# Performance work log

Measured on AMD Instinct MI355X. Metric: run time of the kernel, lower is better.

The kernel has to match this reference:

```python
import jax, jax.numpy as jnp
import numpy as np

LN_EPS = 1e-5


def setup_inputs() -> dict:
    key = jax.random.key(0)
    ks = jax.random.split(key, 10)
    N, E, D, H = 32000, 512000, 256, 128
    atom_features = jax.random.normal(ks[0], (N, D), dtype=jnp.float32)
    edge_features = jax.random.normal(ks[1], (E, H), dtype=jnp.float32)
    edge_index = jax.random.randint(ks[2], (2, E), 0, N, dtype=jnp.int64)
    s = lambda fan_in: 1.0 / np.sqrt(fan_in)
    W_lin = jax.random.normal(ks[3], (D, H), dtype=jnp.float32) * s(D)
    W1 = jax.random.normal(ks[4], (3 * H, H), dtype=jnp.float32) * s(3 * H)
    b1 = jnp.zeros((H,), jnp.float32)
    W2 = jax.random.normal(ks[5], (H, H), dtype=jnp.float32) * s(H)
    b2 = jnp.zeros((H,), jnp.float32)
    W3 = jax.random.normal(ks[6], (H, H), dtype=jnp.float32) * s(H)
    b3 = jnp.zeros((H,), jnp.float32)
    gamma = jnp.ones((H,), jnp.float32)
    beta = jnp.zeros((H,), jnp.float32)
    return dict(atom_features=atom_features, edge_features=edge_features,
                edge_index=edge_index, W_lin=W_lin, W1=W1, b1=b1, W2=W2,
                b2=b2, W3=W3, b3=b3, gamma=gamma, beta=beta)


def _layernorm(x, gamma, beta):
    mu = jnp.mean(x, axis=-1, keepdims=True)
    var = jnp.mean((x - mu) ** 2, axis=-1, keepdims=True)
    return (x - mu) * jax.lax.rsqrt(var + LN_EPS) * gamma + beta


def reference(atom_features, edge_features, edge_index, W_lin, W1, b1, W2, b2, W3, b3, gamma, beta):
    # o3.Linear on scalar irreps -> plain bias-free linear: [N, D] @ [D, H]
    atom_scalars = atom_features @ W_lin  # [N, H]
    edge_dst, edge_src = edge_index[0], edge_index[1]
    # gather + concat: [E, 3H]
    edge_in = jnp.concatenate(
        [atom_scalars[edge_dst], atom_scalars[edge_src], edge_features], axis=-1)
    h = jax.nn.relu(edge_in @ W1 + b1)
    h = jax.nn.relu(h @ W2 + b2)
    h = h @ W3 + b3  # [E, H]
    return _layernorm(edge_features + h, gamma, beta)
```

## Files before the change

kernel.cpp:

```cpp
#include <hip/hip_runtime.h>

typedef __attribute__((ext_vector_type(8))) short bf16x8;
typedef __attribute__((ext_vector_type(16))) float f32x16;
typedef __attribute__((ext_vector_type(4))) float f32x4;
typedef __attribute__((ext_vector_type(4))) unsigned u32x4;

#define LN_EPS 1e-5f

__device__ __forceinline__ unsigned short f2bf(float f) {
    unsigned u = __float_as_uint(f);
    unsigned r = (u + 0x7FFFu + ((u >> 16) & 1u)) >> 16;
    return (unsigned short)r;
}

__device__ __forceinline__ unsigned cvt_pk_bf16(float lo, float hi) {
    unsigned r;
    asm("v_cvt_pk_bf16_f32 %0, %1, %2" : "=v"(r) : "v"(lo), "v"(hi));
    return r;
}

__device__ __forceinline__ void permswap(unsigned& a, unsigned& b) {
    asm("v_permlane32_swap_b32 %0, %1" : "+v"(a), "+v"(b));
}

__global__ void prep_weights(const float* __restrict__ W_lin,
                             const float* __restrict__ W1,
                             const float* __restrict__ W2,
                             const float* __restrict__ W3,
                             unsigned short* __restrict__ wt_lin,
                             unsigned short* __restrict__ wimg) {
    int i = blockIdx.x * blockDim.x + threadIdx.x;
    if (i < 128 * 256) {
        int n = i >> 8, k = i & 255;
        wt_lin[n * 256 + k] = f2bf(W_lin[k * 128 + n]);
    } else if (i < 128 * 256 + 5 * 16384) {
        int j = i - 128 * 256;
        int mat = j >> 14, r = j & 16383;
        int jj = r & 7, l = (r >> 3) & 63, ks = (r >> 9) & 7, f = r >> 12;
        int n = 32 * f + (l & 31);
        int k = 16 * ks + 8 * (l >> 5) + jj;
        float v;
        if (mat < 3)       v = W1[(mat * 128 + k) * 128 + n];
        else if (mat == 3) v = W2[k * 128 + n];
        else               v = W3[k * 128 + n];
        wimg[j] = f2bf(v);
    }
}

__global__ void atoms_gemm(const float* __restrict__ af,
                           const unsigned short* __restrict__ wt_lin,
                           unsigned short* __restrict__ atoms_bf,
                           int Natoms) {
    const int wv = threadIdx.x >> 6, lane = threadIdx.x & 63;
    const int l31 = lane & 31, g8 = (lane >> 5) * 8, g4 = (lane >> 5) * 4;
    const int R = blockIdx.x * 128 + wv * 32;

    f32x16 acc[4];
#pragma unroll
    for (int f = 0; f < 4; ++f)
#pragma unroll
        for (int e = 0; e < 16; ++e) acc[f][e] = 0.0f;

    int arow = R + l31;
    if (arow >= Natoms) arow = Natoms - 1;
    const float* ap = af + (size_t)arow * 256;

#pragma unroll
    for (int ks = 0; ks < 16; ++ks) {
        const int k0 = ks * 16 + g8;
        float4 x0 = *(const float4*)(ap + k0);
        float4 x1 = *(const float4*)(ap + k0 + 4);
        bf16x8 a;
        a[0] = (short)f2bf(x0.x); a[1] = (short)f2bf(x0.y);
        a[2] = (short)f2bf(x0.z); a[3] = (short)f2bf(x0.w);
        a[4] = (short)f2bf(x1.x); a[5] = (short)f2bf(x1.y);
        a[6] = (short)f2bf(x1.z); a[7] = (short)f2bf(x1.w);
#pragma unroll
        for (int f = 0; f < 4; ++f) {
            bf16x8 b = *(const bf16x8*)(wt_lin + (32 * f + l31) * 256 + k0);
            acc[f] = __builtin_amdgcn_mfma_f32_32x32x16_bf16(a, b, acc[f], 0, 0, 0);
        }
    }

#pragma unroll
    for (int f = 0; f < 4; ++f) {
        const int col = 32 * f + l31;
#pragma unroll
        for (int r = 0; r < 16; ++r) {
            int row = R + (r & 3) + 8 * (r >> 2) + g4;
            if (row < Natoms) atoms_bf[(size_t)row * 128 + col] = f2bf(acc[f][r]);
        }
    }
}

__global__ __launch_bounds__(512, 2) void edge_fused(
    const float* __restrict__ ef, const int* __restrict__ eidx,
    const unsigned short* __restrict__ atoms_bf,
    const unsigned short* __restrict__ wimg,
    const float* __restrict__ b1, const float* __restrict__ b2,
    const float* __restrict__ b3, const float* __restrict__ gamma_,
    const float* __restrict__ beta_, float* __restrict__ out, int E) {
    __shared__ unsigned short wlds[4 * 16384];

    const int tid = threadIdx.x;
    const int lane = tid & 63, wv = tid >> 6;
    const int l31 = lane & 31, hi = lane >> 5, h8 = hi * 8;

    {
        const char* s = (const char*)wimg;
        char* d = (char*)wlds;
        const int o = tid * 16;
#pragma unroll
        for (int i = 0; i < 16; ++i)
            __builtin_amdgcn_global_load_lds(
                (const __attribute__((address_space(1))) unsigned int*)(s + o + i * 8192),
                (__attribute__((address_space(3))) unsigned int*)(d + o + i * 8192),
                16, 0, 0);
    }

    const int e0a = blockIdx.x * 512 + wv * 64 + l31;
    const int e0b = e0a + 32;
    const int ea = e0a < E ? e0a : E - 1;
    const int eb = e0b < E ? e0b : E - 1;
    const int dA = eidx[ea], sA = eidx[E + ea];
    const int dB = eidx[eb], sB = eidx[E + eb];
    const unsigned short* dRowA = atoms_bf + (size_t)dA * 128;
    const unsigned short* sRowA = atoms_bf + (size_t)sA * 128;
    const unsigned short* dRowB = atoms_bf + (size_t)dB * 128;
    const unsigned short* sRowB = atoms_bf + (size_t)sB * 128;
    const float* efA = ef + (size_t)ea * 128;
    const float* efB = ef + (size_t)eb * 128;

    bf16x8 gdA[8], gdB[8];
#pragma unroll
    for (int ks = 0; ks < 8; ++ks) {
        gdA[ks] = *(const bf16x8*)(dRowA + ks * 16 + h8);
        gdB[ks] = *(const bf16x8*)(dRowB + ks * 16 + h8);
    }

    f32x16 accA[4], accB[4];
    auto initb = [&](const float* __restrict__ bb) {
#pragma unroll
        for (int f = 0; f < 4; ++f)
#pragma unroll
            for (int m = 0; m < 4; ++m) {
                f32x4 b4 = *(const f32x4*)(bb + 32 * f + 8 * m + 4 * hi);
#pragma unroll
                for (int i = 0; i < 4; ++i) {
                    accA[f][4 * m + i] = b4[i];
                    accB[f][4 * m + i] = b4[i];
                }
            }
    };

    auto build_frags = [&](f32x16* acc, bf16x8* frag) {
#pragma unroll
        for (int f = 0; f < 4; ++f) {
            unsigned pk0[4], pk1[4];
#pragma unroll
            for (int m = 0; m < 4; ++m) {
                float a0 = fmaxf(acc[f][4 * m + 0], 0.0f);
                float a1 = fmaxf(acc[f][4 * m + 1], 0.0f);
                float a2 = fmaxf(acc[f][4 * m + 2], 0.0f);
                float a3 = fmaxf(acc[f][4 * m + 3], 0.0f);
                pk0[m] = cvt_pk_bf16(a0, a1);
                pk1[m] = cvt_pk_bf16(a2, a3);
            }
#pragma unroll
            for (int k1 = 0; k1 < 2; ++k1) {
                unsigned x0 = pk0[2 * k1], y0 = pk0[2 * k1 + 1];
                unsigned x1 = pk1[2 * k1], y1 = pk1[2 * k1 + 1];
                permswap(x0, y0);
                permswap(x1, y1);
                union { u32x4 u; bf16x8 b; } cv;
                cv.u = (u32x4){x0, x1, y0, y1};
                frag[2 * f + k1] = cv.b;
            }
        }
    };

    const unsigned short* lbase = wlds + lane * 8;

    __syncthreads();

    initb(b1);
#pragma unroll
    for (int ks = 0; ks < 8; ++ks) {
#pragma unroll
        for (int f = 0; f < 4; ++f) {
            bf16x8 a = *(const bf16x8*)(lbase + ((0 * 4 + f) * 8 + ks) * 512);
            accA[f] = __builtin_amdgcn_mfma_f32_32x32x16_bf16(a, gdA[ks], accA[f], 0, 0, 0);
            accB[f] = __builtin_amdgcn_mfma_f32_32x32x16_bf16(a, gdB[ks], accB[f], 0, 0, 0);
        }
    }
#pragma unroll
    for (int ks = 0; ks < 8; ++ks) {
        bf16x8 bA = *(const bf16x8*)(sRowA + ks * 16 + h8);
        bf16x8 bB = *(const bf16x8*)(sRowB + ks * 16 + h8);
#pragma unroll
        for (int f = 0; f < 4; ++f) {
            bf16x8 a = *(const bf16x8*)(lbase + ((1 * 4 + f) * 8 + ks) * 512);
            accA[f] = __builtin_amdgcn_mfma_f32_32x32x16_bf16(a, bA, accA[f], 0, 0, 0);
            accB[f] = __builtin_amdgcn_mfma_f32_32x32x16_bf16(a, bB, accB[f], 0, 0, 0);
        }
    }
#pragma unroll
    for (int ks = 0; ks < 8; ++ks) {
        f32x4 xa0 = *(const f32x4*)(efA + ks * 16 + h8);
        f32x4 xa1 = *(const f32x4*)(efA + ks * 16 + h8 + 4);
        f32x4 xb0 = *(const f32x4*)(efB + ks * 16 + h8);
        f32x4 xb1 = *(const f32x4*)(efB + ks * 16 + h8 + 4);
        union { u32x4 u; bf16x8 b; } ca, cb;
        ca.u = (u32x4){cvt_pk_bf16(xa0[0], xa0[1]), cvt_pk_bf16(xa0[2], xa0[3]),
                       cvt_pk_bf16(xa1[0], xa1[1]), cvt_pk_bf16(xa1[2], xa1[3])};
        cb.u = (u32x4){cvt_pk_bf16(xb0[0], xb0[1]), cvt_pk_bf16(xb0[2], xb0[3]),
                       cvt_pk_bf16(xb1[0], xb1[1]), cvt_pk_bf16(xb1[2], xb1[3])};
#pragma unroll
        for (int f = 0; f < 4; ++f) {
            bf16x8 a = *(const bf16x8*)(lbase + ((2 * 4 + f) * 8 + ks) * 512);
            accA[f] = __builtin_amdgcn_mfma_f32_32x32x16_bf16(a, ca.b, accA[f], 0, 0, 0);
            accB[f] = __builtin_amdgcn_mfma_f32_32x32x16_bf16(a, cb.b, accB[f], 0, 0, 0);
        }
    }

    bf16x8 frA[8], frB[8];
    build_frags(accA, frA);
    build_frags(accB, frB);
    initb(b2);
#pragma unroll
    for (int ks = 0; ks < 8; ++ks)
#pragma unroll
        for (int f = 0; f < 4; ++f) {
            bf16x8 a = *(const bf16x8*)(lbase + ((3 * 4 + f) * 8 + ks) * 512);
            accA[f] = __builtin_amdgcn_mfma_f32_32x32x16_bf16(a, frA[ks], accA[f], 0, 0, 0);
            accB[f] = __builtin_amdgcn_mfma_f32_32x32x16_bf16(a, frB[ks], accB[f], 0, 0, 0);
        }

    build_frags(accA, frA);
    build_frags(accB, frB);
    initb(b3);
    const unsigned short* wg3 = wimg + 4 * 16384 + lane * 8;
#pragma unroll
    for (int ks = 0; ks < 8; ++ks)
#pragma unroll
        for (int f = 0; f < 4; ++f) {
            bf16x8 a = *(const bf16x8*)(wg3 + (f * 8 + ks) * 512);
            accA[f] = __builtin_amdgcn_mfma_f32_32x32x16_bf16(a, frA[ks], accA[f], 0, 0, 0);
            accB[f] = __builtin_amdgcn_mfma_f32_32x32x16_bf16(a, frB[ks], accB[f], 0, 0, 0);
        }

    auto epilogue = [&](f32x16* acc, const float* efRow, int e0) {
        float s = 0.0f, q = 0.0f;
#pragma unroll
        for (int f = 0; f < 4; ++f)
#pragma unroll
            for (int m = 0; m < 4; ++m) {
                f32x4 r4 = *(const f32x4*)(efRow + 32 * f + 8 * m + 4 * hi);
#pragma unroll
                for (int i = 0; i < 4; ++i) {
                    float v = acc[f][4 * m + i] + r4[i];
                    acc[f][4 * m + i] = v;
                    s += v;
                    q += v * v;
                }
            }
        s += __shfl_xor(s, 32, 64);
        q += __shfl_xor(q, 32, 64);
        const float mu = s * (1.0f / 128.0f);
        const float var = q * (1.0f / 128.0f) - mu * mu;
        const float rs = rsqrtf(var + LN_EPS);
        if (e0 < E) {
            float* orow = out + (size_t)e0 * 128;
#pragma unroll
            for (int f = 0; f < 4; ++f)
#pragma unroll
                for (int m = 0; m < 4; ++m) {
                    f32x4 g4 = *(const f32x4*)(gamma_ + 32 * f + 8 * m + 4 * hi);
                    f32x4 be4 = *(const f32x4*)(beta_ + 32 * f + 8 * m + 4 * hi);
                    f32x4 o;
#pragma unroll
                    for (int i = 0; i < 4; ++i)
                        o[i] = (acc[f][4 * m + i] - mu) * rs * g4[i] + be4[i];
                    *(f32x4*)(orow + 32 * f + 8 * m + 4 * hi) = o;
                }
        }
    };
    epilogue(accA, efA, e0a);
    epilogue(accB, efB, e0b);
}

extern "C" void kernel_launch(void* const* d_in, const int* in_sizes, int n_in,
                              void* d_out, int out_size, void* d_ws, size_t ws_size,
                              hipStream_t stream) {
    const float* atom_features = (const float*)d_in[0];
    const float* edge_features = (const float*)d_in[1];
    const int* edge_index = (const int*)d_in[2];
    const float* W_lin = (const float*)d_in[3];
    const float* W1 = (const float*)d_in[4];
    const float* b1 = (const float*)d_in[5];
    const float* W2 = (const float*)d_in[6];
    const float* b2 = (const float*)d_in[7];
    const float* W3 = (const float*)d_in[8];
    const float* b3 = (const float*)d_in[9];
    const float* gamma_ = (const float*)d_in[10];
    const float* beta_ = (const float*)d_in[11];
    float* out = (float*)d_out;

    const int Natoms = in_sizes[0] / 256;
    const int E = in_sizes[1] / 128;

    unsigned short* atoms_bf = (unsigned short*)d_ws;
    unsigned short* wt_lin = atoms_bf + (size_t)Natoms * 128;
    unsigned short* wimg = wt_lin + 128 * 256;

    const int prep_items = 128 * 256 + 5 * 16384;
    prep_weights<<<(prep_items + 255) / 256, 256, 0, stream>>>(W_lin, W1, W2, W3,
                                                               wt_lin, wimg);
    atoms_gemm<<<(Natoms + 127) / 128, 256, 0, stream>>>(atom_features, wt_lin,
                                                         atoms_bf, Natoms);
    edge_fused<<<(E + 511) / 512, 512, 0, stream>>>(edge_features, edge_index,
                                                    atoms_bf, wimg, b1, b2, b3,
                                                    gamma_, beta_, out, E);
}
```

Baseline: 266.8 us.

## Make edge kernel persistent and prefetch next tile's gathered rows

Turns the edge kernel into a persistent grid of at most 256 blocks that loop over 512-edge tiles. Each block loads the weights into LDS only once, and while computing the current tile it fetches the next tile's edge indices and destination-row gathers. This amortizes the weight staging and hides gather latency behind MFMA work. The cost is fewer resident blocks: 256 blocks at two per CU may underfill the GPU, and prefetch registers add pressure.

```diff
diff --git a/kernel.cpp b/kernel.cpp
--- a/kernel.cpp
+++ b/kernel.cpp
@@ -99,7 +99,7 @@
     const unsigned short* __restrict__ wimg,
     const float* __restrict__ b1, const float* __restrict__ b2,
     const float* __restrict__ b3, const float* __restrict__ gamma_,
-    const float* __restrict__ beta_, float* __restrict__ out, int E) {
+    const float* __restrict__ beta_, float* __restrict__ out, int E, int ntiles) {
     __shared__ unsigned short wlds[4 * 16384];
 
     const int tid = threadIdx.x;
@@ -118,16 +118,30 @@
                 16, 0, 0);
     }
 
-    const int e0a = blockIdx.x * 512 + wv * 64 + l31;
-    const int e0b = e0a + 32;
-    const int ea = e0a < E ? e0a : E - 1;
-    const int eb = e0b < E ? e0b : E - 1;
-    const int dA = eidx[ea], sA = eidx[E + ea];
-    const int dB = eidx[eb], sB = eidx[E + eb];
-    const unsigned short* dRowA = atoms_bf + (size_t)dA * 128;
-    const unsigned short* sRowA = atoms_bf + (size_t)sA * 128;
-    const unsigned short* dRowB = atoms_bf + (size_t)dB * 128;
-    const unsigned short* sRowB = atoms_bf + (size_t)sB * 128;
+    int t = blockIdx.x;
+    if (t >= ntiles) { __syncthreads(); return; }
+
+    auto tile_edges = [&](int tt, int& e0a, int& e0b, int& ea, int& eb) {
+        e0a = tt * 512 + wv * 64 + l31;
+        e0b = e0a + 32;
+        ea = e0a < E ? e0a : E - 1;
+        eb = e0b < E ? e0b : E - 1;
+    };
+
+    int e0a, e0b, ea, eb;
+    tile_edges(t, e0a, e0b, ea, eb);
+    const unsigned short* sRowA;
+    const unsigned short* sRowB;
+    const unsigned short* dRowA;
+    const unsigned short* dRowB;
+    {
+        int dA = eidx[ea], sA = eidx[E + ea];
+        int dB = eidx[eb], sB = eidx[E + eb];
+        dRowA = atoms_bf + (size_t)dA * 128;
+        sRowA = atoms_bf + (size_t)sA * 128;
+        dRowB = atoms_bf + (size_t)dB * 128;
+        sRowB = atoms_bf + (size_t)sB * 128;
+    }
     const float* efA = ef + (size_t)ea * 128;
     const float* efB = ef + (size_t)eb * 128;
 
@@ -179,76 +193,6 @@
         }
     };
 
-    const unsigned short* lbase = wlds + lane * 8;
-
-    __syncthreads();
-
-    initb(b1);
-#pragma unroll
-    for (int ks = 0; ks < 8; ++ks) {
-#pragma unroll
-        for (int f = 0; f < 4; ++f) {
-            bf16x8 a = *(const bf16x8*)(lbase + ((0 * 4 + f) * 8 + ks) * 512);
-            accA[f] = __builtin_amdgcn_mfma_f32_32x32x16_bf16(a, gdA[ks], accA[f], 0, 0, 0);
-            accB[f] = __builtin_amdgcn_mfma_f32_32x32x16_bf16(a, gdB[ks], accB[f], 0, 0, 0);
-        }
-    }
-#pragma unroll
-    for (int ks = 0; ks < 8; ++ks) {
-        bf16x8 bA = *(const bf16x8*)(sRowA + ks * 16 + h8);
-        bf16x8 bB = *(const bf16x8*)(sRowB + ks * 16 + h8);
-#pragma unroll
-        for (int f = 0; f < 4; ++f) {
-            bf16x8 a = *(const bf16x8*)(lbase + ((1 * 4 + f) * 8 + ks) * 512);
-            accA[f] = __builtin_amdgcn_mfma_f32_32x32x16_bf16(a, bA, accA[f], 0, 0, 0);
-            accB[f] = __builtin_amdgcn_mfma_f32_32x32x16_bf16(a, bB, accB[f], 0, 0, 0);
-        }
-    }
-#pragma unroll
-    for (int ks = 0; ks < 8; ++ks) {
-        f32x4 xa0 = *(const f32x4*)(efA + ks * 16 + h8);
-        f32x4 xa1 = *(const f32x4*)(efA + ks * 16 + h8 + 4);
-        f32x4 xb0 = *(const f32x4*)(efB + ks * 16 + h8);
-        f32x4 xb1 = *(const f32x4*)(efB + ks * 16 + h8 + 4);
-        union { u32x4 u; bf16x8 b; } ca, cb;
-        ca.u = (u32x4){cvt_pk_bf16(xa0[0], xa0[1]), cvt_pk_bf16(xa0[2], xa0[3]),
-                       cvt_pk_bf16(xa1[0], xa1[1]), cvt_pk_bf16(xa1[2], xa1[3])};
-        cb.u = (u32x4){cvt_pk_bf16(xb0[0], xb0[1]), cvt_pk_bf16(xb0[2], xb0[3]),
-                       cvt_pk_bf16(xb1[0], xb1[1]), cvt_pk_bf16(xb1[2], xb1[3])};
-#pragma unroll
-        for (int f = 0; f < 4; ++f) {
-            bf16x8 a = *(const bf16x8*)(lbase + ((2 * 4 + f) * 8 + ks) * 512);
-            accA[f] = __builtin_amdgcn_mfma_f32_32x32x16_bf16(a, ca.b, accA[f], 0, 0, 0);
-            accB[f] = __builtin_amdgcn_mfma_f32_32x32x16_bf16(a, cb.b, accB[f], 0, 0, 0);
-        }
-    }
-
-    bf16x8 frA[8], frB[8];
-    build_frags(accA, frA);
-    build_frags(accB, frB);
-    initb(b2);
-#pragma unroll
-    for (int ks = 0; ks < 8; ++ks)
-#pragma unroll
-        for (int f = 0; f < 4; ++f) {
-            bf16x8 a = *(const bf16x8*)(lbase + ((3 * 4 + f) * 8 + ks) * 512);
-            accA[f] = __builtin_amdgcn_mfma_f32_32x32x16_bf16(a, frA[ks], accA[f], 0, 0, 0);
-            accB[f] = __builtin_amdgcn_mfma_f32_32x32x16_bf16(a, frB[ks], accB[f], 0, 0, 0);
-        }
-
-    build_frags(accA, frA);
-    build_frags(accB, frB);
-    initb(b3);
-    const unsigned short* wg3 = wimg + 4 * 16384 + lane * 8;
-#pragma unroll
-    for (int ks = 0; ks < 8; ++ks)
-#pragma unroll
-        for (int f = 0; f < 4; ++f) {
-            bf16x8 a = *(const bf16x8*)(wg3 + (f * 8 + ks) * 512);
-            accA[f] = __builtin_amdgcn_mfma_f32_32x32x16_bf16(a, frA[ks], accA[f], 0, 0, 0);
-            accB[f] = __builtin_amdgcn_mfma_f32_32x32x16_bf16(a, frB[ks], accB[f], 0, 0, 0);
-        }
-
     auto epilogue = [&](f32x16* acc, const float* efRow, int e0) {
         float s = 0.0f, q = 0.0f;
 #pragma unroll
@@ -285,8 +229,115 @@
                 }
         }
     };
-    epilogue(accA, efA, e0a);
-    epilogue(accB, efB, e0b);
+
+    const unsigned short* lbase = wlds + lane * 8;
+    const unsigned short* wg3 = wimg + 4 * 16384 + lane * 8;
+
+    __syncthreads();
+
+    while (true) {
+        const int tn = t + gridDim.x;
+        const bool more = tn < ntiles;
+
+        int e0a_n, e0b_n, ea_n, eb_n;
+        const unsigned short *dRowA_n, *dRowB_n, *sRowA_n, *sRowB_n;
+        const float *efA_n, *efB_n;
+        if (more) {
+            tile_edges(tn, e0a_n, e0b_n, ea_n, eb_n);
+            int dA = eidx[ea_n], sA = eidx[E + ea_n];
+            int dB = eidx[eb_n], sB = eidx[E + eb_n];
+            dRowA_n = atoms_bf + (size_t)dA * 128;
+            sRowA_n = atoms_bf + (size_t)sA * 128;
+            dRowB_n = atoms_bf + (size_t)dB * 128;
+            sRowB_n = atoms_bf + (size_t)sB * 128;
+            efA_n = ef + (size_t)ea_n * 128;
+            efB_n = ef + (size_t)eb_n * 128;
+        }
+
+        initb(b1);
+#pragma unroll
+        for (int ks = 0; ks < 8; ++ks) {
+#pragma unroll
+            for (int f = 0; f < 4; ++f) {
+                bf16x8 a = *(const bf16x8*)(lbase + ((0 * 4 + f) * 8 + ks) * 512);
+                accA[f] = __builtin_amdgcn_mfma_f32_32x32x16_bf16(a, gdA[ks], accA[f], 0, 0, 0);
+                accB[f] = __builtin_amdgcn_mfma_f32_32x32x16_bf16(a, gdB[ks], accB[f], 0, 0, 0);
+            }
+        }
+
+        if (more) {
+#pragma unroll
+            for (int ks = 0; ks < 8; ++ks) {
+                gdA[ks] = *(const bf16x8*)(dRowA_n + ks * 16 + h8);
+                gdB[ks] = *(const bf16x8*)(dRowB_n + ks * 16 + h8);
+            }
+        }
+
+#pragma unroll
+        for (int ks = 0; ks < 8; ++ks) {
+            bf16x8 bA = *(const bf16x8*)(sRowA + ks * 16 + h8);
+            bf16x8 bB = *(const bf16x8*)(sRowB + ks * 16 + h8);
+#pragma unroll
+            for (int f = 0; f < 4; ++f) {
+                bf16x8 a = *(const bf16x8*)(lbase + ((1 * 4 + f) * 8 + ks) * 512);
+                accA[f] = __builtin_amdgcn_mfma_f32_32x32x16_bf16(a, bA, accA[f], 0, 0, 0);
+                accB[f] = __builtin_amdgcn_mfma_f32_32x32x16_bf16(a, bB, accB[f], 0, 0, 0);
+            }
+        }
+
+#pragma unroll
+        for (int ks = 0; ks < 8; ++ks) {
+            f32x4 xa0 = *(const f32x4*)(efA + ks * 16 + h8);
+            f32x4 xa1 = *(const f32x4*)(efA + ks * 16 + h8 + 4);
+            f32x4 xb0 = *(const f32x4*)(efB + ks * 16 + h8);
+            f32x4 xb1 = *(const f32x4*)(efB + ks * 16 + h8 + 4);
+            union { u32x4 u; bf16x8 b; } ca, cb;
+            ca.u = (u32x4){cvt_pk_bf16(xa0[0], xa0[1]), cvt_pk_bf16(xa0[2], xa0[3]),
+                           cvt_pk_bf16(xa1[0], xa1[1]), cvt_pk_bf16(xa1[2], xa1[3])};
+            cb.u = (u32x4){cvt_pk_bf16(xb0[0], xb0[1]), cvt_pk_bf16(xb0[2], xb0[3]),
+                           cvt_pk_bf16(xb1[0], xb1[1]), cvt_pk_bf16(xb1[2], xb1[3])};
+#pragma unroll
+            for (int f = 0; f < 4; ++f) {
+                bf16x8 a = *(const bf16x8*)(lbase + ((2 * 4 + f) * 8 + ks) * 512);
+                accA[f] = __builtin_amdgcn_mfma_f32_32x32x16_bf16(a, ca.b, accA[f], 0, 0, 0);
+                accB[f] = __builtin_amdgcn_mfma_f32_32x32x16_bf16(a, cb.b, accB[f], 0, 0, 0);
+            }
+        }
+
+        bf16x8 frA[8], frB[8];
+        build_frags(accA, frA);
+        build_frags(accB, frB);
+        initb(b2);
+#pragma unroll
+        for (int ks = 0; ks < 8; ++ks)
+#pragma unroll
+            for (int f = 0; f < 4; ++f) {
+                bf16x8 a = *(const bf16x8*)(lbase + ((3 * 4 + f) * 8 + ks) * 512);
+                accA[f] = __builtin_amdgcn_mfma_f32_32x32x16_bf16(a, frA[ks], accA[f], 0, 0, 0);
+                accB[f] = __builtin_amdgcn_mfma_f32_32x32x16_bf16(a, frB[ks], accB[f], 0, 0, 0);
+            }
+
+        build_frags(accA, frA);
+        build_frags(accB, frB);
+        initb(b3);
+#pragma unroll
+        for (int ks = 0; ks < 8; ++ks)
+#pragma unroll
+            for (int f = 0; f < 4; ++f) {
+                bf16x8 a = *(const bf16x8*)(wg3 + (f * 8 + ks) * 512);
+                accA[f] = __builtin_amdgcn_mfma_f32_32x32x16_bf16(a, frA[ks], accA[f], 0, 0, 0);
+                accB[f] = __builtin_amdgcn_mfma_f32_32x32x16_bf16(a, frB[ks], accB[f], 0, 0, 0);
+            }
+
+        epilogue(accA, efA, e0a);
+        epilogue(accB, efB, e0b);
+
+        if (!more) break;
+        t = tn;
+        e0a = e0a_n; e0b = e0b_n;
+        sRowA = sRowA_n; sRowB = sRowB_n;
+        efA = efA_n; efB = efB_n;
+    }
 }
 
 extern "C" void kernel_launch(void* const* d_in, const int* in_sizes, int n_in,
@@ -318,7 +369,9 @@
                                                                wt_lin, wimg);
     atoms_gemm<<<(Natoms + 127) / 128, 256, 0, stream>>>(atom_features, wt_lin,
                                                          atoms_bf, Natoms);
-    edge_fused<<<(E + 511) / 512, 512, 0, stream>>>(edge_features, edge_index,
-                                                    atoms_bf, wimg, b1, b2, b3,
-                                                    gamma_, beta_, out, E);
-}
+    const int ntiles = (E + 511) / 512;
+    const int nblk = ntiles < 256 ? ntiles : 256;
+    edge_fused<<<nblk, 512, 0, stream>>>(edge_features, edge_index,
+                                         atoms_bf, wimg, b1, b2, b3,
+                                         gamma_, beta_, out, E, ntiles);
+}
```

New measurement: 680.9 us. +155.2%, slower.
